# Optimization experiments

Measured on AMD Instinct MI355X. Metric: run time of the kernel, lower is better.

The kernel has to match this reference:

```python
import jax, jax.numpy as jnp
import numpy as np

D_MODEL = 1024
N_HEADS = 16
D_HEAD = D_MODEL // N_HEADS


def setup_inputs() -> dict:
    key = jax.random.key(0)
    kx, kq, kk, kv, ko = jax.random.split(key, 5)
    s = 1.0 / np.sqrt(D_MODEL)  # ~ nn.Linear init scale
    return {
        "x": jax.random.normal(kx, (2, 2048, D_MODEL), dtype=jnp.float32),
        "Wq": jax.random.uniform(kq, (D_MODEL, D_MODEL), jnp.float32, -s, s),
        "Wk": jax.random.uniform(kk, (D_MODEL, D_MODEL), jnp.float32, -s, s),
        "Wv": jax.random.uniform(kv, (D_MODEL, D_MODEL), jnp.float32, -s, s),
        "Wo": jax.random.uniform(ko, (D_MODEL, D_MODEL), jnp.float32, -s, s),
    }


def reference(x, Wq, Wk, Wv, Wo):
    B, T, D = x.shape
    H, Dh = N_HEADS, D_HEAD
    # nn.Linear computes x @ W.T; project then split heads -> [B,H,T,Dh]
    q = (x @ Wq.T).reshape(B, T, H, Dh).transpose(0, 2, 1, 3)
    k = (x @ Wk.T).reshape(B, T, H, Dh).transpose(0, 2, 1, 3)
    v = (x @ Wv.T).reshape(B, T, H, Dh).transpose(0, 2, 1, 3)
    att = jnp.einsum("bhqd,bhkd->bhqk", q, k) / jnp.sqrt(jnp.float32(Dh))
    causal = jnp.tril(jnp.ones((T, T), dtype=bool))  # True = keep
    att = jnp.where(causal[None, None], att, -jnp.inf)
    w = jax.nn.softmax(att, axis=-1)
    out = jnp.einsum("bhqk,bhkd->bhqd", w, v)
    out = out.transpose(0, 2, 1, 3).reshape(B, T, D)
    return out @ Wo.T
```

## Files before the change

kernel.cpp:

```cpp
#include <hip/hip_runtime.h>
#include <hip/hip_bf16.h>

typedef __bf16 bf16;
typedef __bf16 bf16x4 __attribute__((ext_vector_type(4)));
typedef __bf16 bf16x8 __attribute__((ext_vector_type(8)));
typedef float  f32x4  __attribute__((ext_vector_type(4)));

#define DEV static __device__ __forceinline__

DEV void gload_lds16(const void* g, void* l) {
  __builtin_amdgcn_global_load_lds((const __attribute__((address_space(1))) void*)g,
                                   (__attribute__((address_space(3))) void*)l, 16, 0, 0);
}

DEV f32x4 mfma16(bf16x8 a, bf16x8 b, f32x4 c) {
  return __builtin_amdgcn_mfma_f32_16x16x32_bf16(a, b, c, 0, 0, 0);
}

__global__ void convert_all(const float* __restrict__ x,
                            const float* __restrict__ wq, const float* __restrict__ wk,
                            const float* __restrict__ wv, const float* __restrict__ wo,
                            bf16* __restrict__ xb,
                            bf16* __restrict__ wqb, bf16* __restrict__ wkb,
                            bf16* __restrict__ wvb, bf16* __restrict__ wob) {
  const int NX = 4194304;
  const int NW = 1048576;
  const int total4 = (NX + 4 * NW) / 4;
  for (int i = blockIdx.x * blockDim.x + threadIdx.x; i < total4;
       i += gridDim.x * blockDim.x) {
    int e = i * 4;
    const float* src; bf16* dst; int off;
    if (e < NX) { src = x; dst = xb; off = e; }
    else {
      int r = e - NX; int w = r >> 20; off = r & (NW - 1);
      src = (w == 0) ? wq : (w == 1) ? wk : (w == 2) ? wv : wo;
      dst = (w == 0) ? wqb : (w == 1) ? wkb : (w == 2) ? wvb : wob;
    }
    float4 v = *(const float4*)(src + off);
    bf16x4 o; o[0] = (bf16)v.x; o[1] = (bf16)v.y; o[2] = (bf16)v.z; o[3] = (bf16)v.w;
    *(bf16x4*)(dst + off) = o;
  }
}

__global__ __launch_bounds__(256) void gemm_qkv(const bf16* __restrict__ xb,
                                                const bf16* __restrict__ Wq_,
                                                const bf16* __restrict__ Wk_,
                                                const bf16* __restrict__ Wv_,
                                                bf16* __restrict__ Qg,
                                                bf16* __restrict__ Kg,
                                                bf16* __restrict__ Vtg) {
  const int z = blockIdx.z;
  const bf16* A  = (z == 2) ? Wv_ : xb;
  const bf16* Bw = (z == 0) ? Wq_ : (z == 1) ? Wk_ : xb;
  const int K = 1024;
  __shared__ bf16 As[128 * 32];
  __shared__ bf16 Bs[128 * 32];
  const int tid = threadIdx.x, w = tid >> 6, l = tid & 63;
  const int row0 = (z == 2 ? blockIdx.y : blockIdx.x) * 128;
  const int col0 = (z == 2 ? blockIdx.x : blockIdx.y) * 128;
  const int wr = (w >> 1) * 64, wc = (w & 1) * 64;
  const int lr = l & 15, lg = l >> 4;
  const int srow = l >> 2, scol = (l & 3) * 8;
  f32x4 acc[4][4] = {};

  for (int kt = 0; kt < 32; ++kt) {
    const int k0 = kt * 32;
#pragma unroll
    for (int i = 0; i < 2; ++i) {
      const int chunk = w * 2 + i;
      gload_lds16(A  + (row0 + chunk * 16 + srow) * K + k0 + scol, &As[chunk * 512]);
      gload_lds16(Bw + (col0 + chunk * 16 + srow) * K + k0 + scol, &Bs[chunk * 512]);
    }
    __syncthreads();
    bf16x8 af[4], bfr[4];
#pragma unroll
    for (int m = 0; m < 4; ++m) af[m]  = *(const bf16x8*)&As[(wr + m * 16 + lr) * 32 + lg * 8];
#pragma unroll
    for (int n = 0; n < 4; ++n) bfr[n] = *(const bf16x8*)&Bs[(wc + n * 16 + lr) * 32 + lg * 8];
#pragma unroll
    for (int m = 0; m < 4; ++m)
#pragma unroll
      for (int n = 0; n < 4; ++n)
        acc[m][n] = mfma16(af[m], bfr[n], acc[m][n]);
    __syncthreads();
  }

  if (z == 2) {
#pragma unroll
    for (int m = 0; m < 4; ++m)
#pragma unroll
      for (int n = 0; n < 4; ++n)
#pragma unroll
        for (int e = 0; e < 4; ++e) {
          const int rr = row0 + wr + m * 16 + lg * 4 + e;
          const int cc = col0 + wc + n * 16 + lr;
          const int h = rr >> 6, dh = rr & 63;
          const int b = cc >> 11, t = cc & 2047;
          Vtg[(((size_t)(b * 16 + h) * 64) + dh) * 2048 + t] = (bf16)acc[m][n][e];
        }
  } else {
    const float scl = (z == 0) ? 0.18033688011112042f : 1.0f;
    bf16* out = (z == 0) ? Qg : Kg;
#pragma unroll
    for (int m = 0; m < 4; ++m)
#pragma unroll
      for (int n = 0; n < 4; ++n)
#pragma unroll
        for (int e = 0; e < 4; ++e) {
          const int r = row0 + wr + m * 16 + lg * 4 + e;
          const int c = col0 + wc + n * 16 + lr;
          const int b = r >> 11, t = r & 2047;
          const int h = c >> 6,  dh = c & 63;
          out[(((size_t)(b * 16 + h) * 2048) + t) * 64 + dh] = (bf16)(acc[m][n][e] * scl);
        }
  }
}

__global__ __launch_bounds__(256) void attn(const bf16* __restrict__ Qg,
                                            const bf16* __restrict__ Kg,
                                            const bf16* __restrict__ Vtg,
                                            bf16* __restrict__ Obt) {
  const int id  = blockIdx.y * 16 + blockIdx.x;
  const int swz = (id & 7) * 64 + (id >> 3);
  const int bh  = swz >> 4;
  const int x   = swz & 15;
  const int tid = threadIdx.x, w = tid >> 6, l = tid & 63;
  const int lr = l & 15, lg = l >> 4;
  __shared__ bf16 Ks[2][4096];
  __shared__ bf16 Vs[2][4096];
  __shared__ bf16 Ps[4][1024];
  const size_t base = (size_t)bh * 2048 * 64;
  const char* kbase = (const char*)(Kg + base);
  const char* vbase = (const char*)(Vtg + base);

  const int rA0 = x * 64 + w * 16;
  const int rB0 = (31 - x) * 64 + w * 16;

  bf16x8 qA[2], qB[2];
  {
    const bf16* qp = Qg + base + (size_t)(rA0 + lr) * 64;
    qA[0] = *(const bf16x8*)(qp + lg * 8);
    qA[1] = *(const bf16x8*)(qp + 32 + lg * 8);
    const bf16* qq = Qg + base + (size_t)(rB0 + lr) * 64;
    qB[0] = *(const bf16x8*)(qq + lg * 8);
    qB[1] = *(const bf16x8*)(qq + 32 + lg * 8);
  }
  f32x4 oA[4] = {}, oB[4] = {};
  f32x4 lA = {}, lB = {};

  bf16x8 ones;
#pragma unroll
  for (int j = 0; j < 8; ++j) ones[j] = (bf16)1.0f;

  const int cxor = lr & 7;

  auto stage = [&](int kt, int buf) {
#pragma unroll
    for (int i = 0; i < 2; ++i) {
      const int p = (w * 2 + i) * 1024 + l * 16;
      const int sw = p ^ (((p >> 7) & 7) << 4);
      gload_lds16(kbase + (size_t)kt * 8192 + sw, &Ks[buf][(w * 2 + i) * 512]);
      const int vrow = p >> 7;
      const int vcol = (p & 127) ^ (((p >> 7) & 7) << 4);
      gload_lds16(vbase + (size_t)vrow * 4096 + kt * 128 + vcol,
                  &Vs[buf][(w * 2 + i) * 512]);
    }
  };

  auto computeTile = [&](int kt, int buf, int myrow0, bf16x8 (&qf)[2],
                         f32x4 (&acco)[4], f32x4& lacc) {
    const int k0 = kt * 64;
    const bool full = (k0 + 63 <= myrow0);
    f32x4 accs[4] = {};
    __builtin_amdgcn_s_setprio(1);
#pragma unroll
    for (int n = 0; n < 4; ++n) {
      const int r = n * 16 + lr;
      bf16x8 kf0 = *(const bf16x8*)&Ks[buf][(r * 128 + ((lg ^ cxor) << 4)) / 2];
      bf16x8 kf1 = *(const bf16x8*)&Ks[buf][(r * 128 + (((4 + lg) ^ cxor) << 4)) / 2];
      accs[n] = mfma16(kf0, qf[0], accs[n]);
      accs[n] = mfma16(kf1, qf[1], accs[n]);
    }
    __builtin_amdgcn_s_setprio(0);
    if (!full) {
      const int q = myrow0 + lr;
#pragma unroll
      for (int n = 0; n < 4; ++n) {
        const int keyb = k0 + n * 16 + lg * 4;
#pragma unroll
        for (int e = 0; e < 4; ++e)
          if (keyb + e > q) accs[n][e] = -__builtin_inff();
      }
    }
#pragma unroll
    for (int n = 0; n < 4; ++n)
#pragma unroll
      for (int e = 0; e < 4; ++e) accs[n][e] = exp2f(accs[n][e]);
#pragma unroll
    for (int n = 0; n < 4; ++n) {
      bf16x4 p4;
#pragma unroll
      for (int e = 0; e < 4; ++e) p4[e] = (bf16)accs[n][e];
      const int off = (lr * 128 + (n * 16 + lg * 4) * 2) ^ ((lr & 7) << 4);
      *(bf16x4*)((char*)Ps[w] + off) = p4;
    }
    __builtin_amdgcn_s_setprio(1);
#pragma unroll
    for (int c = 0; c < 2; ++c) {
      bf16x8 pf = *(const bf16x8*)((char*)Ps[w] +
                    (lr * 128 + (((c * 4 + lg) ^ cxor) << 4)));
      lacc = mfma16(pf, ones, lacc);
#pragma unroll
      for (int n = 0; n < 4; ++n) {
        const int r = n * 16 + lr;
        bf16x8 vf = *(const bf16x8*)&Vs[buf][(r * 128 + (((c * 4 + lg) ^ cxor) << 4)) / 2];
        acco[n] = mfma16(pf, vf, acco[n]);
      }
    }
    __builtin_amdgcn_s_setprio(0);
  };

  const int nkt = 32 - x;
  stage(0, 0);
  int cur = 0;
  for (int kt = 0; kt < nkt; ++kt) {
    __syncthreads();
    if (kt + 1 < nkt) stage(kt + 1, cur ^ 1);
    if (kt <= x)
      computeTile(kt, cur, rA0, qA, oA, lA);
    computeTile(kt, cur, rB0, qB, oB, lB);
    cur ^= 1;
  }

  const int b = bh >> 4, h = bh & 15;
  f32x4 invA, invB;
#pragma unroll
  for (int e = 0; e < 4; ++e) {
    invA[e] = __builtin_amdgcn_rcpf(lA[e]);
    invB[e] = __builtin_amdgcn_rcpf(lB[e]);
  }
#pragma unroll
  for (int n = 0; n < 4; ++n)
#pragma unroll
    for (int e = 0; e < 4; ++e) {
      const int rA = rA0 + lg * 4 + e;
      Obt[((size_t)(b * 2048 + rA)) * 1024 + h * 64 + n * 16 + lr] = (bf16)(oA[n][e] * invA[e]);
      const int rB = rB0 + lg * 4 + e;
      Obt[((size_t)(b * 2048 + rB)) * 1024 + h * 64 + n * 16 + lr] = (bf16)(oB[n][e] * invB[e]);
    }
}

__global__ __launch_bounds__(256) void gemm_out(const bf16* __restrict__ A,
                                                const bf16* __restrict__ Bw,
                                                float* __restrict__ Cout) {
  const int K = 1024;
  __shared__ bf16 As[128 * 32];
  __shared__ bf16 Bs[128 * 32];
  const int tid = threadIdx.x, w = tid >> 6, l = tid & 63;
  const int row0 = blockIdx.x * 128, col0 = blockIdx.y * 128;
  const int wr = (w >> 1) * 64, wc = (w & 1) * 64;
  const int lr = l & 15, lg = l >> 4;
  const int srow = l >> 2, scol = (l & 3) * 8;
  f32x4 acc[4][4] = {};

  for (int kt = 0; kt < 32; ++kt) {
    const int k0 = kt * 32;
#pragma unroll
    for (int i = 0; i < 2; ++i) {
      const int chunk = w * 2 + i;
      gload_lds16(A  + (row0 + chunk * 16 + srow) * K + k0 + scol, &As[chunk * 512]);
      gload_lds16(Bw + (col0 + chunk * 16 + srow) * K + k0 + scol, &Bs[chunk * 512]);
    }
    __syncthreads();
    bf16x8 af[4], bfr[4];
#pragma unroll
    for (int m = 0; m < 4; ++m) af[m]  = *(const bf16x8*)&As[(wr + m * 16 + lr) * 32 + lg * 8];
#pragma unroll
    for (int n = 0; n < 4; ++n) bfr[n] = *(const bf16x8*)&Bs[(wc + n * 16 + lr) * 32 + lg * 8];
#pragma unroll
    for (int m = 0; m < 4; ++m)
#pragma unroll
      for (int n = 0; n < 4; ++n)
        acc[m][n] = mfma16(af[m], bfr[n], acc[m][n]);
    __syncthreads();
  }

#pragma unroll
  for (int m = 0; m < 4; ++m)
#pragma unroll
    for (int n = 0; n < 4; ++n)
#pragma unroll
      for (int e = 0; e < 4; ++e) {
        const int r = row0 + wr + m * 16 + lg * 4 + e;
        const int c = col0 + wc + n * 16 + lr;
        Cout[(size_t)r * 1024 + c] = acc[m][n][e];
      }
}

extern "C" void kernel_launch(void* const* d_in, const int* in_sizes, int n_in,
                              void* d_out, int out_size, void* d_ws, size_t ws_size,
                              hipStream_t stream) {
  const float* x  = (const float*)d_in[0];
  const float* wq = (const float*)d_in[1];
  const float* wk = (const float*)d_in[2];
  const float* wv = (const float*)d_in[3];
  const float* wo = (const float*)d_in[4];
  float* out = (float*)d_out;

  bf16* xb  = (bf16*)d_ws;
  bf16* wqb = xb  + 4194304;
  bf16* wkb = wqb + 1048576;
  bf16* wvb = wkb + 1048576;
  bf16* wob = wvb + 1048576;
  bf16* Qg  = wob + 1048576;
  bf16* Kg  = Qg  + 4194304;
  bf16* Vtg = Kg  + 4194304;
  bf16* Obt = Vtg + 4194304;

  convert_all<<<2048, 256, 0, stream>>>(x, wq, wk, wv, wo, xb, wqb, wkb, wvb, wob);
  gemm_qkv<<<dim3(32, 8, 3), 256, 0, stream>>>(xb, wqb, wkb, wvb, Qg, Kg, Vtg);
  attn<<<dim3(16, 32), 256, 0, stream>>>(Qg, Kg, Vtg, Obt);
  gemm_out<<<dim3(32, 8), 256, 0, stream>>>(Obt, wob, out);
}
```

Measured before the change: 118.3 us.

## Use BK=64 XOR-swizzled LDS tiles in GEMMs and shrink out-proj tile

Both projection GEMMs now stage 64-wide K slices into LDS through a row-XOR swizzle, which halves the number of K iterations and barriers and is meant to avoid LDS bank conflicts on the 16-byte fragment reads. The output-projection GEMM moves to 128x64 tiles, doubling its grid to 512 blocks so the CUs are better filled. The trade-off is more LDS per block, which may lower occupancy, and less reuse per block in the output GEMM.

```diff
diff --git a/kernel.cpp b/kernel.cpp
--- a/kernel.cpp
+++ b/kernel.cpp
@@ -42,6 +42,15 @@
   }
 }
 
+DEV void stage_tile64(const bf16* gsrc, int grow0, int gcol0, int ld_elems,
+                      bf16* lds, int chunk, int l) {
+  const int p = chunk * 1024 + l * 16;
+  const int r = p >> 7;
+  const int cb = (p & 127) ^ ((r & 7) << 4);
+  gload_lds16((const char*)gsrc + ((size_t)(grow0 + r) * ld_elems + gcol0) * 2 + cb,
+              (char*)lds + p);
+}
+
 __global__ __launch_bounds__(256) void gemm_qkv(const bf16* __restrict__ xb,
                                                 const bf16* __restrict__ Wq_,
                                                 const bf16* __restrict__ Wk_,
@@ -53,35 +62,47 @@
   const bf16* A  = (z == 2) ? Wv_ : xb;
   const bf16* Bw = (z == 0) ? Wq_ : (z == 1) ? Wk_ : xb;
   const int K = 1024;
-  __shared__ bf16 As[128 * 32];
-  __shared__ bf16 Bs[128 * 32];
+  __shared__ bf16 As[128 * 64];
+  __shared__ bf16 Bs[128 * 64];
   const int tid = threadIdx.x, w = tid >> 6, l = tid & 63;
   const int row0 = (z == 2 ? blockIdx.y : blockIdx.x) * 128;
   const int col0 = (z == 2 ? blockIdx.x : blockIdx.y) * 128;
   const int wr = (w >> 1) * 64, wc = (w & 1) * 64;
   const int lr = l & 15, lg = l >> 4;
-  const int srow = l >> 2, scol = (l & 3) * 8;
+  const int cxor = lr & 7;
   f32x4 acc[4][4] = {};
 
-  for (int kt = 0; kt < 32; ++kt) {
-    const int k0 = kt * 32;
-#pragma unroll
-    for (int i = 0; i < 2; ++i) {
-      const int chunk = w * 2 + i;
-      gload_lds16(A  + (row0 + chunk * 16 + srow) * K + k0 + scol, &As[chunk * 512]);
-      gload_lds16(Bw + (col0 + chunk * 16 + srow) * K + k0 + scol, &Bs[chunk * 512]);
-    }
-    __syncthreads();
-    bf16x8 af[4], bfr[4];
-#pragma unroll
-    for (int m = 0; m < 4; ++m) af[m]  = *(const bf16x8*)&As[(wr + m * 16 + lr) * 32 + lg * 8];
-#pragma unroll
-    for (int n = 0; n < 4; ++n) bfr[n] = *(const bf16x8*)&Bs[(wc + n * 16 + lr) * 32 + lg * 8];
+  for (int kt = 0; kt < 16; ++kt) {
+    const int k0 = kt * 64;
+#pragma unroll
+    for (int i = 0; i < 4; ++i) {
+      const int chunk = w * 4 + i;
+      stage_tile64(A,  row0, k0, K, As, chunk, l);
+      stage_tile64(Bw, col0, k0, K, Bs, chunk, l);
+    }
+    __syncthreads();
+    bf16x8 af[4][2], bfr[4][2];
+#pragma unroll
+    for (int m = 0; m < 4; ++m) {
+      const int r = wr + m * 16 + lr;
+#pragma unroll
+      for (int h = 0; h < 2; ++h)
+        af[m][h] = *(const bf16x8*)((char*)As + r * 128 + (((h * 4 + lg) ^ cxor) << 4));
+    }
+#pragma unroll
+    for (int n = 0; n < 4; ++n) {
+      const int r = wc + n * 16 + lr;
+#pragma unroll
+      for (int h = 0; h < 2; ++h)
+        bfr[n][h] = *(const bf16x8*)((char*)Bs + r * 128 + (((h * 4 + lg) ^ cxor) << 4));
+    }
 #pragma unroll
     for (int m = 0; m < 4; ++m)
 #pragma unroll
-      for (int n = 0; n < 4; ++n)
-        acc[m][n] = mfma16(af[m], bfr[n], acc[m][n]);
+      for (int n = 0; n < 4; ++n) {
+        acc[m][n] = mfma16(af[m][0], bfr[n][0], acc[m][n]);
+        acc[m][n] = mfma16(af[m][1], bfr[n][1], acc[m][n]);
+      }
     __syncthreads();
   }
 
@@ -254,41 +275,53 @@
                                                 const bf16* __restrict__ Bw,
                                                 float* __restrict__ Cout) {
   const int K = 1024;
-  __shared__ bf16 As[128 * 32];
-  __shared__ bf16 Bs[128 * 32];
+  __shared__ bf16 As[128 * 64];
+  __shared__ bf16 Bs[64 * 64];
   const int tid = threadIdx.x, w = tid >> 6, l = tid & 63;
-  const int row0 = blockIdx.x * 128, col0 = blockIdx.y * 128;
-  const int wr = (w >> 1) * 64, wc = (w & 1) * 64;
+  const int row0 = blockIdx.x * 128, col0 = blockIdx.y * 64;
+  const int wr = (w >> 1) * 64, wc = (w & 1) * 32;
   const int lr = l & 15, lg = l >> 4;
-  const int srow = l >> 2, scol = (l & 3) * 8;
-  f32x4 acc[4][4] = {};
-
-  for (int kt = 0; kt < 32; ++kt) {
-    const int k0 = kt * 32;
-#pragma unroll
-    for (int i = 0; i < 2; ++i) {
-      const int chunk = w * 2 + i;
-      gload_lds16(A  + (row0 + chunk * 16 + srow) * K + k0 + scol, &As[chunk * 512]);
-      gload_lds16(Bw + (col0 + chunk * 16 + srow) * K + k0 + scol, &Bs[chunk * 512]);
-    }
-    __syncthreads();
-    bf16x8 af[4], bfr[4];
-#pragma unroll
-    for (int m = 0; m < 4; ++m) af[m]  = *(const bf16x8*)&As[(wr + m * 16 + lr) * 32 + lg * 8];
-#pragma unroll
-    for (int n = 0; n < 4; ++n) bfr[n] = *(const bf16x8*)&Bs[(wc + n * 16 + lr) * 32 + lg * 8];
+  const int cxor = lr & 7;
+  f32x4 acc[4][2] = {};
+
+  for (int kt = 0; kt < 16; ++kt) {
+    const int k0 = kt * 64;
+#pragma unroll
+    for (int i = 0; i < 4; ++i)
+      stage_tile64(A, row0, k0, K, As, w * 4 + i, l);
+#pragma unroll
+    for (int i = 0; i < 2; ++i)
+      stage_tile64(Bw, col0, k0, K, Bs, w * 2 + i, l);
+    __syncthreads();
+    bf16x8 af[4][2], bfr[2][2];
+#pragma unroll
+    for (int m = 0; m < 4; ++m) {
+      const int r = wr + m * 16 + lr;
+#pragma unroll
+      for (int h = 0; h < 2; ++h)
+        af[m][h] = *(const bf16x8*)((char*)As + r * 128 + (((h * 4 + lg) ^ cxor) << 4));
+    }
+#pragma unroll
+    for (int n = 0; n < 2; ++n) {
+      const int r = wc + n * 16 + lr;
+#pragma unroll
+      for (int h = 0; h < 2; ++h)
+        bfr[n][h] = *(const bf16x8*)((char*)Bs + r * 128 + (((h * 4 + lg) ^ cxor) << 4));
+    }
 #pragma unroll
     for (int m = 0; m < 4; ++m)
 #pragma unroll
-      for (int n = 0; n < 4; ++n)
-        acc[m][n] = mfma16(af[m], bfr[n], acc[m][n]);
+      for (int n = 0; n < 2; ++n) {
+        acc[m][n] = mfma16(af[m][0], bfr[n][0], acc[m][n]);
+        acc[m][n] = mfma16(af[m][1], bfr[n][1], acc[m][n]);
+      }
     __syncthreads();
   }
 
 #pragma unroll
   for (int m = 0; m < 4; ++m)
 #pragma unroll
-    for (int n = 0; n < 4; ++n)
+    for (int n = 0; n < 2; ++n)
 #pragma unroll
       for (int e = 0; e < 4; ++e) {
         const int r = row0 + wr + m * 16 + lg * 4 + e;
@@ -320,5 +353,5 @@
   convert_all<<<2048, 256, 0, stream>>>(x, wq, wk, wv, wo, xb, wqb, wkb, wvb, wob);
   gemm_qkv<<<dim3(32, 8, 3), 256, 0, stream>>>(xb, wqb, wkb, wvb, Qg, Kg, Vtg);
   attn<<<dim3(16, 32), 256, 0, stream>>>(Qg, Kg, Vtg, Obt);
-  gemm_out<<<dim3(32, 8), 256, 0, stream>>>(Obt, wob, out);
-}
+  gemm_out<<<dim3(32, 16), 256, 0, stream>>>(Obt, wob, out);
+}
```

After: 111.4 us. -5.8%, faster.
